# Kernel tuning notes

Measured on AMD Instinct MI355X. Metric: run time of the kernel, lower is better.

## Reference

```python
import jax, jax.numpy as jnp
import numpy as np

N = 1024  # batch rows; each row has 480 features

def setup_inputs() -> dict:
    key = jax.random.key(0)
    kx, kS, kT, kH, kL = jax.random.split(key, 5)
    x = jax.random.normal(kx, (N, 480), dtype=jnp.float32)
    S = jax.random.normal(kS, (30, 2, 15), dtype=jnp.float32)    # buffer
    T = jax.random.normal(kT, (30, 15), dtype=jnp.float32)       # param
    H = jax.random.normal(kH, (45, 4096), dtype=jnp.float32)     # buffer (hash matrix)
    LUT = jax.random.normal(kL, (10, 4096, 2), dtype=jnp.float32)  # param (codebook)
    return {"x": x, "S": S, "T": T, "H": H, "LUT": LUT}

def reference(x, S, T, H, LUT):
    # (N, 480) -> (N, 8, 30, 2)
    x4 = x.reshape(-1, 8, 30, 2)
    # project each 2-vector through S: (N, 8, 30, 15)
    y = jnp.einsum('abcd,cdk->abck', x4, S) - T - 1e-4
    # straight-through sign-tanh binarization
    tanh = jnp.tanh(y)
    y = jax.lax.stop_gradient(jnp.sign(y) - tanh) + tanh
    # (N, 8, 10, 45): 30*15 = 10*(3*15)
    y = y.reshape(-1, 8, 10, 45)
    # hash scores over 4096 codes: (N, 8, 10, 4096)
    scores = jnp.einsum('bpcd,dk->bpck', y, H)
    idx = jnp.argmax(scores, axis=-1)  # (N, 8, 10) int
    # one_hot @ LUT is exactly a gather: out[b,p,c,:] = LUT[c, idx[b,p,c], :]
    out = LUT[jnp.arange(10)[None, None, :], idx]  # (N, 8, 10, 2)
    return out
```

## Files before the change

kernel.cpp:

```cpp
#include <hip/hip_runtime.h>
#include <math.h>

#define M_ROWS  81920
#define NCOLS   4096
#define KPAD    48
#define NCHUNK  4
#define CHUNKC  (NCOLS / NCHUNK)
#define CROUNDS (CHUNKC / 32)
#define GROUNDS (NCOLS / 32)
#define FRAG    512
#define ROUNDH  (3 * FRAG)
#define LO_SCALE 4096.0f
#define INV_LO   (1.0f / 4096.0f)

typedef _Float16 f16x8  __attribute__((ext_vector_type(8)));
typedef float    f32x16 __attribute__((ext_vector_type(16)));


__global__ void build_B_kernel(const float* __restrict__ H,
                               _Float16* __restrict__ Bhi_pk,
                               _Float16* __restrict__ Blo_pk) {
    const int n = blockIdx.x * 256 + threadIdx.x;
    const int r = n >> 5;
    const int l = n & 31;
    float hi[KPAD], lo[KPAD];
    #pragma unroll
    for (int k = 0; k < 45; ++k) {
        const float h = H[k * NCOLS + n];
        const _Float16 h1 = (_Float16)h;
        hi[k] = (float)h1;
        lo[k] = (h - (float)h1) * LO_SCALE;
    }
    #pragma unroll
    for (int k = 45; k < KPAD; ++k) { hi[k] = 0.f; lo[k] = 0.f; }
    #pragma unroll
    for (int kt = 0; kt < 3; ++kt) {
        f16x8 h0, h1v, l0, l1v;
        #pragma unroll
        for (int j = 0; j < 8; ++j) {
            h0[j]  = (_Float16)hi[kt * 16 + j];
            h1v[j] = (_Float16)hi[kt * 16 + 8 + j];
            l0[j]  = (_Float16)lo[kt * 16 + j];
            l1v[j] = (_Float16)lo[kt * 16 + 8 + j];
        }
        _Float16* dh = Bhi_pk + (size_t)(r * 3 + kt) * FRAG;
        _Float16* dl = Blo_pk + (size_t)(r * 3 + kt) * FRAG;
        *(f16x8*)(dh + l * 8)        = h0;
        *(f16x8*)(dh + (l + 32) * 8) = h1v;
        *(f16x8*)(dl + l * 8)        = l0;
        *(f16x8*)(dl + (l + 32) * 8) = l1v;
    }
}

__global__ __launch_bounds__(256, 2) void score_argmax_kernel(
        const float* __restrict__ x,
        const float* __restrict__ S,
        const float* __restrict__ T,
        const _Float16* __restrict__ Bhi_pk,
        const _Float16* __restrict__ Blo_pk,
        float* __restrict__ pbest,
        int*   __restrict__ pidx) {
    const int tid  = threadIdx.x;
    const int lane = tid & 63;
    const int l31  = lane & 31;
    const int half = lane >> 5;
    const int chunk = blockIdx.x / 320;
    const int rg    = (blockIdx.x - chunk * 320) * 4 + (tid >> 6);
    const int rowbase = rg * 64;

    f16x8 afr[2][3];
    #pragma unroll
    for (int rt = 0; rt < 2; ++rt) {
        const int row  = rowbase + rt * 32 + l31;
        const int pair = row / 10;
        const int c2   = row - pair * 10;
        const int a    = pair >> 3;
        const int b    = pair & 7;
        const float* xp = x + a * 480 + b * 60;
        #pragma unroll
        for (int kt = 0; kt < 3; ++kt) {
            #pragma unroll
            for (int j = 0; j < 8; ++j) {
                const int k    = kt * 16 + half * 8 + j;
                const bool pad = (k >= 45);
                const int kcl  = pad ? 0 : k;
                const int cc   = kcl / 15;
                const int kk   = kcl - cc * 15;
                const int c    = c2 * 3 + cc;
                const float x0 = xp[c * 2 + 0];
                const float x1 = xp[c * 2 + 1];
                float v = x0 * S[(c * 2 + 0) * 15 + kk] + x1 * S[(c * 2 + 1) * 15 + kk];
                v = v - T[c * 15 + kk] - 1e-4f;
                const float yv = (v > 0.f) ? 1.f : ((v < 0.f) ? -1.f : 0.f);
                afr[rt][kt][j] = pad ? (_Float16)0.f : (_Float16)yv;
            }
        }
    }

    float best[2][16];
    int   bidx[2][16];
    #pragma unroll
    for (int rt = 0; rt < 2; ++rt)
        #pragma unroll
        for (int e = 0; e < 16; ++e) { best[rt][e] = -INFINITY; bidx[rt][e] = 0; }

    const int colbase0 = chunk * CHUNKC;
    const _Float16* hbase = Bhi_pk + (size_t)(chunk * CROUNDS) * ROUNDH + lane * 8;
    const _Float16* lbase = Blo_pk + (size_t)(chunk * CROUNDS) * ROUNDH + lane * 8;

    f16x8 cb[6], nb[6];
    #pragma unroll
    for (int kt = 0; kt < 3; ++kt) {
        cb[kt]     = *(const f16x8*)(hbase + kt * FRAG);
        cb[3 + kt] = *(const f16x8*)(lbase + kt * FRAG);
    }

    for (int ct = 0; ct < CROUNDS; ++ct) {
        {
            const _Float16* hp = hbase + (size_t)(ct + 1) * ROUNDH;
            const _Float16* lp = lbase + (size_t)(ct + 1) * ROUNDH;
            #pragma unroll
            for (int kt = 0; kt < 3; ++kt) {
                nb[kt]     = *(const f16x8*)(hp + kt * FRAG);
                nb[3 + kt] = *(const f16x8*)(lp + kt * FRAG);
            }
        }
        const int mycol = colbase0 + ct * 32 + l31;
        #pragma unroll
        for (int rt = 0; rt < 2; ++rt) {
            f32x16 ch; f32x16 cl;
            #pragma unroll
            for (int e = 0; e < 16; ++e) { ch[e] = 0.f; cl[e] = 0.f; }
            ch = __builtin_amdgcn_mfma_f32_32x32x16_f16(afr[rt][0], cb[0], ch, 0, 0, 0);
            ch = __builtin_amdgcn_mfma_f32_32x32x16_f16(afr[rt][1], cb[1], ch, 0, 0, 0);
            ch = __builtin_amdgcn_mfma_f32_32x32x16_f16(afr[rt][2], cb[2], ch, 0, 0, 0);
            cl = __builtin_amdgcn_mfma_f32_32x32x16_f16(afr[rt][0], cb[3], cl, 0, 0, 0);
            cl = __builtin_amdgcn_mfma_f32_32x32x16_f16(afr[rt][1], cb[4], cl, 0, 0, 0);
            cl = __builtin_amdgcn_mfma_f32_32x32x16_f16(afr[rt][2], cb[5], cl, 0, 0, 0);
            #pragma unroll
            for (int e = 0; e < 16; ++e) {
                const float s = fmaf(cl[e], INV_LO, ch[e]);
                if (s > best[rt][e]) bidx[rt][e] = mycol;
                best[rt][e] = fmaxf(best[rt][e], s);
            }
        }
        #pragma unroll
        for (int q = 0; q < 6; ++q) cb[q] = nb[q];
    }

    #pragma unroll
    for (int m = 1; m < 32; m <<= 1) {
        #pragma unroll
        for (int rt = 0; rt < 2; ++rt)
            #pragma unroll
            for (int e = 0; e < 16; ++e) {
                const float ov = __shfl_xor(best[rt][e], m, 64);
                const int   oi = __shfl_xor(bidx[rt][e], m, 64);
                if (ov > best[rt][e] ||
                    (ov == best[rt][e] && oi < bidx[rt][e])) {
                    best[rt][e] = ov; bidx[rt][e] = oi;
                }
            }
    }

    if (l31 == 0) {
        #pragma unroll
        for (int rt = 0; rt < 2; ++rt)
            #pragma unroll
            for (int e = 0; e < 16; ++e) {
                const int row = rowbase + rt * 32 + (e & 3) + 8 * (e >> 2) + 4 * half;
                pbest[(size_t)row * NCHUNK + chunk] = best[rt][e];
                pidx [(size_t)row * NCHUNK + chunk] = bidx[rt][e];
            }
    }
}

__global__ void reduce_lut_kernel(const float* __restrict__ pbest,
                                  const int*   __restrict__ pidx,
                                  const float* __restrict__ LUT,
                                  float* __restrict__ out) {
    const int row = blockIdx.x * blockDim.x + threadIdx.x;
    if (row >= M_ROWS) return;
    float best = -INFINITY;
    int   bi   = 0;
    #pragma unroll
    for (int ch = 0; ch < NCHUNK; ++ch) {
        const float bv = pbest[(size_t)row * NCHUNK + ch];
        const int   ix = pidx [(size_t)row * NCHUNK + ch];
        if (bv > best) { best = bv; bi = ix; }
    }
    const int pair = row / 10;
    const int c2   = row - pair * 10;
    const float* l = LUT + ((size_t)c2 * NCOLS + bi) * 2;
    out[row * 2 + 0] = l[0];
    out[row * 2 + 1] = l[1];
}

extern "C" void kernel_launch(void* const* d_in, const int* in_sizes, int n_in,
                              void* d_out, int out_size, void* d_ws, size_t ws_size,
                              hipStream_t stream) {
    const float* x   = (const float*)d_in[0];
    const float* S   = (const float*)d_in[1];
    const float* T   = (const float*)d_in[2];
    const float* H   = (const float*)d_in[3];
    const float* LUT = (const float*)d_in[4];
    float* out = (float*)d_out;

    _Float16* Bhi_pk = (_Float16*)d_ws;
    _Float16* Blo_pk = Bhi_pk + (size_t)GROUNDS * ROUNDH;
    float*  pbest = (float*)(Blo_pk + (size_t)GROUNDS * ROUNDH);
    int*    pidx  = (int*)(pbest + (size_t)M_ROWS * NCHUNK);

    build_B_kernel<<<16, 256, 0, stream>>>(H, Bhi_pk, Blo_pk);
    score_argmax_kernel<<<1280, 256, 0, stream>>>(x, S, T, Bhi_pk, Blo_pk, pbest, pidx);
    reduce_lut_kernel<<<M_ROWS / 256, 256, 0, stream>>>(pbest, pidx, LUT, out);
}
```

Baseline: 194.3 us.

## Process one 32-row tile per wave and drop B-fragment prefetch

Each wave now handles 32 rows instead of 64, and the grid doubles to 2560 blocks. The software prefetch of the next round's B fragments is removed, so B is loaded right before it is used. This cuts register pressure (fewer accumulators and fragments) and may allow more waves per CU. The cost is half the reuse of each B load across rows, which doubles global/L2 traffic for B, and global load latency is no longer hidden by explicit prefetch.

```diff
diff --git a/kernel.cpp b/kernel.cpp
--- a/kernel.cpp
+++ b/kernel.cpp
@@ -64,14 +64,13 @@
     const int lane = tid & 63;
     const int l31  = lane & 31;
     const int half = lane >> 5;
-    const int chunk = blockIdx.x / 320;
-    const int rg    = (blockIdx.x - chunk * 320) * 4 + (tid >> 6);
-    const int rowbase = rg * 64;
+    const int chunk = blockIdx.x / 640;
+    const int rg    = (blockIdx.x - chunk * 640) * 4 + (tid >> 6);
+    const int rowbase = rg * 32;
 
-    f16x8 afr[2][3];
-    #pragma unroll
-    for (int rt = 0; rt < 2; ++rt) {
-        const int row  = rowbase + rt * 32 + l31;
+    f16x8 afr[3];
+    {
+        const int row  = rowbase + l31;
         const int pair = row / 10;
         const int c2   = row - pair * 10;
         const int a    = pair >> 3;
@@ -92,86 +91,68 @@
                 float v = x0 * S[(c * 2 + 0) * 15 + kk] + x1 * S[(c * 2 + 1) * 15 + kk];
                 v = v - T[c * 15 + kk] - 1e-4f;
                 const float yv = (v > 0.f) ? 1.f : ((v < 0.f) ? -1.f : 0.f);
-                afr[rt][kt][j] = pad ? (_Float16)0.f : (_Float16)yv;
+                afr[kt][j] = pad ? (_Float16)0.f : (_Float16)yv;
             }
         }
     }
 
-    float best[2][16];
-    int   bidx[2][16];
+    float best[16];
+    int   bidx[16];
     #pragma unroll
-    for (int rt = 0; rt < 2; ++rt)
-        #pragma unroll
-        for (int e = 0; e < 16; ++e) { best[rt][e] = -INFINITY; bidx[rt][e] = 0; }
+    for (int e = 0; e < 16; ++e) { best[e] = -INFINITY; bidx[e] = 0; }
 
     const int colbase0 = chunk * CHUNKC;
     const _Float16* hbase = Bhi_pk + (size_t)(chunk * CROUNDS) * ROUNDH + lane * 8;
     const _Float16* lbase = Blo_pk + (size_t)(chunk * CROUNDS) * ROUNDH + lane * 8;
 
-    f16x8 cb[6], nb[6];
-    #pragma unroll
-    for (int kt = 0; kt < 3; ++kt) {
-        cb[kt]     = *(const f16x8*)(hbase + kt * FRAG);
-        cb[3 + kt] = *(const f16x8*)(lbase + kt * FRAG);
-    }
+    for (int ct = 0; ct < CROUNDS; ++ct) {
+        const _Float16* hp = hbase + (size_t)ct * ROUNDH;
+        const _Float16* lp = lbase + (size_t)ct * ROUNDH;
+        const f16x8 bh0 = *(const f16x8*)(hp);
+        const f16x8 bh1 = *(const f16x8*)(hp + FRAG);
+        const f16x8 bh2 = *(const f16x8*)(hp + 2 * FRAG);
+        const f16x8 bl0 = *(const f16x8*)(lp);
+        const f16x8 bl1 = *(const f16x8*)(lp + FRAG);
+        const f16x8 bl2 = *(const f16x8*)(lp + 2 * FRAG);
 
-    for (int ct = 0; ct < CROUNDS; ++ct) {
-        {
-            const _Float16* hp = hbase + (size_t)(ct + 1) * ROUNDH;
-            const _Float16* lp = lbase + (size_t)(ct + 1) * ROUNDH;
-            #pragma unroll
-            for (int kt = 0; kt < 3; ++kt) {
-                nb[kt]     = *(const f16x8*)(hp + kt * FRAG);
-                nb[3 + kt] = *(const f16x8*)(lp + kt * FRAG);
-            }
-        }
+        f32x16 ch; f32x16 cl;
+        #pragma unroll
+        for (int e = 0; e < 16; ++e) { ch[e] = 0.f; cl[e] = 0.f; }
+        ch = __builtin_amdgcn_mfma_f32_32x32x16_f16(afr[0], bh0, ch, 0, 0, 0);
+        ch = __builtin_amdgcn_mfma_f32_32x32x16_f16(afr[1], bh1, ch, 0, 0, 0);
+        ch = __builtin_amdgcn_mfma_f32_32x32x16_f16(afr[2], bh2, ch, 0, 0, 0);
+        cl = __builtin_amdgcn_mfma_f32_32x32x16_f16(afr[0], bl0, cl, 0, 0, 0);
+        cl = __builtin_amdgcn_mfma_f32_32x32x16_f16(afr[1], bl1, cl, 0, 0, 0);
+        cl = __builtin_amdgcn_mfma_f32_32x32x16_f16(afr[2], bl2, cl, 0, 0, 0);
+
         const int mycol = colbase0 + ct * 32 + l31;
         #pragma unroll
-        for (int rt = 0; rt < 2; ++rt) {
-            f32x16 ch; f32x16 cl;
-            #pragma unroll
-            for (int e = 0; e < 16; ++e) { ch[e] = 0.f; cl[e] = 0.f; }
-            ch = __builtin_amdgcn_mfma_f32_32x32x16_f16(afr[rt][0], cb[0], ch, 0, 0, 0);
-            ch = __builtin_amdgcn_mfma_f32_32x32x16_f16(afr[rt][1], cb[1], ch, 0, 0, 0);
-            ch = __builtin_amdgcn_mfma_f32_32x32x16_f16(afr[rt][2], cb[2], ch, 0, 0, 0);
-            cl = __builtin_amdgcn_mfma_f32_32x32x16_f16(afr[rt][0], cb[3], cl, 0, 0, 0);
-            cl = __builtin_amdgcn_mfma_f32_32x32x16_f16(afr[rt][1], cb[4], cl, 0, 0, 0);
-            cl = __builtin_amdgcn_mfma_f32_32x32x16_f16(afr[rt][2], cb[5], cl, 0, 0, 0);
-            #pragma unroll
-            for (int e = 0; e < 16; ++e) {
-                const float s = fmaf(cl[e], INV_LO, ch[e]);
-                if (s > best[rt][e]) bidx[rt][e] = mycol;
-                best[rt][e] = fmaxf(best[rt][e], s);
-            }
+        for (int e = 0; e < 16; ++e) {
+            const float s = fmaf(cl[e], INV_LO, ch[e]);
+            if (s > best[e]) bidx[e] = mycol;
+            best[e] = fmaxf(best[e], s);
         }
-        #pragma unroll
-        for (int q = 0; q < 6; ++q) cb[q] = nb[q];
     }
 
     #pragma unroll
     for (int m = 1; m < 32; m <<= 1) {
         #pragma unroll
-        for (int rt = 0; rt < 2; ++rt)
-            #pragma unroll
-            for (int e = 0; e < 16; ++e) {
-                const float ov = __shfl_xor(best[rt][e], m, 64);
-                const int   oi = __shfl_xor(bidx[rt][e], m, 64);
-                if (ov > best[rt][e] ||
-                    (ov == best[rt][e] && oi < bidx[rt][e])) {
-                    best[rt][e] = ov; bidx[rt][e] = oi;
-                }
+        for (int e = 0; e < 16; ++e) {
+            const float ov = __shfl_xor(best[e], m, 64);
+            const int   oi = __shfl_xor(bidx[e], m, 64);
+            if (ov > best[e] || (ov == best[e] && oi < bidx[e])) {
+                best[e] = ov; bidx[e] = oi;
             }
+        }
     }
 
     if (l31 == 0) {
         #pragma unroll
-        for (int rt = 0; rt < 2; ++rt)
-            #pragma unroll
-            for (int e = 0; e < 16; ++e) {
-                const int row = rowbase + rt * 32 + (e & 3) + 8 * (e >> 2) + 4 * half;
-                pbest[(size_t)row * NCHUNK + chunk] = best[rt][e];
-                pidx [(size_t)row * NCHUNK + chunk] = bidx[rt][e];
-            }
+        for (int e = 0; e < 16; ++e) {
+            const int row = rowbase + (e & 3) + 8 * (e >> 2) + 4 * half;
+            pbest[(size_t)row * NCHUNK + chunk] = best[e];
+            pidx [(size_t)row * NCHUNK + chunk] = bidx[e];
+        }
     }
 }
 
@@ -212,6 +193,6 @@
     int*    pidx  = (int*)(pbest + (size_t)M_ROWS * NCHUNK);
 
     build_B_kernel<<<16, 256, 0, stream>>>(H, Bhi_pk, Blo_pk);
-    score_argmax_kernel<<<1280, 256, 0, stream>>>(x, S, T, Bhi_pk, Blo_pk, pbest, pidx);
+    score_argmax_kernel<<<2560, 256, 0, stream>>>(x, S, T, Bhi_pk, Blo_pk, pbest, pidx);
     reduce_lut_kernel<<<M_ROWS / 256, 256, 0, stream>>>(pbest, pidx, LUT, out);
 }
```

Result: slower. 212.8 us (+9.5%).
